# Kernel tuning notes

Hardware: AMD Instinct MI355X
Metric: run time of the kernel (lower is better)

## Reference

```python
import jax, jax.numpy as jnp
import numpy as np

N = 100000          # nodes
E = 1600000         # edges
NODE_DIM = 128
EDGE_DIM = 1
EMB = 16            # out_channels per head
H = 2               # heads
HID = 32
OUT = 2
NEG_SLOPE = 0.2


def gatv2_layer(x, src, dst, eattr, Wl, bl, Wr, br, We, att, bias):
    """PyG GATv2Conv: add self-loops (edge_attr fill='mean'), edge attention,
    segment softmax over target nodes, scatter-add aggregation, concat heads."""
    n = x.shape[0]
    heads, ch = att.shape
    # --- add self loops; self-loop edge_attr = mean of incoming edge_attr per node ---
    ones = jnp.ones((src.shape[0],), dtype=x.dtype)
    deg = jax.ops.segment_sum(ones, dst, num_segments=n)
    loop_attr = jax.ops.segment_sum(eattr, dst, num_segments=n) / jnp.maximum(deg, 1.0)[:, None]
    idx = jnp.arange(n, dtype=src.dtype)
    src2 = jnp.concatenate([src, idx])
    dst2 = jnp.concatenate([dst, idx])
    eattr2 = jnp.concatenate([eattr, loop_attr], axis=0)
    # --- linear projections ---
    xl = (x @ Wl + bl).reshape(n, heads, ch)   # source-side (lin_l)
    xr = (x @ Wr + br).reshape(n, heads, ch)   # target-side (lin_r)
    ef = (eattr2 @ We).reshape(-1, heads, ch)  # edge features (lin_edge, no bias)
    # --- per-edge attention logits (GATv2: LeakyReLU inside, then att dot) ---
    e = xl[src2] + xr[dst2] + ef               # [E2, H, C]
    e = jnp.where(e >= 0, e, NEG_SLOPE * e)
    logits = jnp.einsum('ehc,hc->eh', e, att)  # [E2, H]
    # --- segment softmax over edges sharing the same target node ---
    m = jax.ops.segment_max(logits, dst2, num_segments=n)      # [N, H]
    a = jnp.exp(logits - m[dst2])
    denom = jax.ops.segment_sum(a, dst2, num_segments=n)
    alpha = a / denom[dst2]                                    # [E2, H]
    # --- scatter-add weighted source messages ---
    msg = (alpha[:, :, None] * xl[src2]).reshape(-1, heads * ch)
    out = jax.ops.segment_sum(msg, dst2, num_segments=n)       # [N, H*C]
    return out + bias


def setup_inputs() -> dict:
    key = jax.random.key(0)
    ks = jax.random.split(key, 24)
    p = lambda k, s: (jax.random.normal(k, s, dtype=jnp.float32) * 0.1)
    HC = H * EMB
    return {
        'x': jax.random.normal(ks[0], (N, NODE_DIM), dtype=jnp.float32),
        'edge_index': jax.random.randint(ks[1], (2, E), 0, N, dtype=jnp.int32),
        'edge_attr': jax.random.normal(ks[2], (E, EDGE_DIM), dtype=jnp.float32),
        # layer 1
        'Wl1': p(ks[3], (NODE_DIM, HC)), 'bl1': p(ks[4], (HC,)),
        'Wr1': p(ks[5], (NODE_DIM, HC)), 'br1': p(ks[6], (HC,)),
        'We1': p(ks[7], (EDGE_DIM, HC)), 'att1': p(ks[8], (H, EMB)), 'b1': p(ks[9], (HC,)),
        # layer 2 (input dim = H*EMB)
        'Wl2': p(ks[10], (HC, HC)), 'bl2': p(ks[11], (HC,)),
        'Wr2': p(ks[12], (HC, HC)), 'br2': p(ks[13], (HC,)),
        'We2': p(ks[14], (EDGE_DIM, HC)), 'att2': p(ks[15], (H, EMB)), 'b2': p(ks[16], (HC,)),
        # decoder MLP
        'Wd1': p(ks[17], (HC, HID)), 'bd1': p(ks[18], (HID,)),
        'Wd2': p(ks[19], (HID, OUT)), 'bd2': p(ks[20], (OUT,)),
    }


def reference(x, edge_index, edge_attr,
              Wl1, bl1, Wr1, br1, We1, att1, b1,
              Wl2, bl2, Wr2, br2, We2, att2, b2,
              Wd1, bd1, Wd2, bd2):
    src, dst = edge_index[0], edge_index[1]
    h = gatv2_layer(x, src, dst, edge_attr, Wl1, bl1, Wr1, br1, We1, att1, b1)
    h = gatv2_layer(h, src, dst, edge_attr, Wl2, bl2, Wr2, br2, We2, att2, b2)
    h = jax.nn.relu(h @ Wd1 + bd1)
    return h @ Wd2 + bd2
```

## Files before the change

### kernel.cpp

```cpp
#include <hip/hip_runtime.h>
#include <hip/hip_fp16.h>
#include <math.h>


#define NN 100000
#define NE 1600000
#define SLOT 48
#define ROWU 64
#define NEG_SLOPE 0.2f

__global__ void scatter_kernel(const int* __restrict__ src, const int* __restrict__ dst,
                               const float* __restrict__ eattr,
                               unsigned* __restrict__ csr) {
    int e = blockIdx.x * blockDim.x + threadIdx.x;
    if (e >= NE) return;
    int d = dst[e];
    unsigned* row = csr + (size_t)d * ROWU;
    int pos = atomicAdd((int*)row, 1);
    if (pos < SLOT) {
        unsigned hb = __half_as_ushort(__float2half_rn(eattr[e]));
        row[4 + pos] = ((unsigned)src[e] << 15) | (hb >> 1);
    }
}

__device__ __forceinline__ int pk_src(unsigned p) { return (int)(p >> 15); }
__device__ __forceinline__ float pk_ea(unsigned p) {
    return __half2float(__ushort_as_half((unsigned short)((p & 0x7FFFu) << 1)));
}

template <int K>
__global__ void proj_kernel(const float* __restrict__ x,
                            const float* __restrict__ Wl, const float* __restrict__ bl,
                            const float* __restrict__ Wr, const float* __restrict__ br,
                            __half* __restrict__ xl, float* __restrict__ xr) {
    __shared__ float sWl[K * 32];
    __shared__ float sWr[K * 32];
    __shared__ float sb[64];
    for (int i = threadIdx.x; i < K * 32; i += blockDim.x) {
        sWl[i] = Wl[i];
        sWr[i] = Wr[i];
    }
    if (threadIdx.x < 32) sb[threadIdx.x] = bl[threadIdx.x];
    else if (threadIdx.x < 64) sb[threadIdx.x] = br[threadIdx.x - 32];
    __syncthreads();
    int t = blockIdx.x * blockDim.x + threadIdx.x;
    int g = t >> 5, col = t & 31;
    int row0 = g * 2;
    if (row0 >= NN) return;
    const float4* xr0 = (const float4*)(x + (size_t)row0 * K);
    const float4* xr1 = (const float4*)(x + (size_t)(row0 + 1) * K);
    float al0 = 0.f, ar0 = 0.f, al1 = 0.f, ar1 = 0.f;
#pragma unroll
    for (int k4 = 0; k4 < K / 4; k4++) {
        float4 a = xr0[k4];
        float4 b = xr1[k4];
        int k = k4 * 4;
        float wl0 = sWl[(k + 0) * 32 + col], wr0 = sWr[(k + 0) * 32 + col];
        float wl1 = sWl[(k + 1) * 32 + col], wr1 = sWr[(k + 1) * 32 + col];
        float wl2 = sWl[(k + 2) * 32 + col], wr2 = sWr[(k + 2) * 32 + col];
        float wl3 = sWl[(k + 3) * 32 + col], wr3 = sWr[(k + 3) * 32 + col];
        al0 = fmaf(a.x, wl0, al0); ar0 = fmaf(a.x, wr0, ar0);
        al1 = fmaf(b.x, wl0, al1); ar1 = fmaf(b.x, wr0, ar1);
        al0 = fmaf(a.y, wl1, al0); ar0 = fmaf(a.y, wr1, ar0);
        al1 = fmaf(b.y, wl1, al1); ar1 = fmaf(b.y, wr1, ar1);
        al0 = fmaf(a.z, wl2, al0); ar0 = fmaf(a.z, wr2, ar0);
        al1 = fmaf(b.z, wl2, al1); ar1 = fmaf(b.z, wr2, ar1);
        al0 = fmaf(a.w, wl3, al0); ar0 = fmaf(a.w, wr3, ar0);
        al1 = fmaf(b.w, wl3, al1); ar1 = fmaf(b.w, wr3, ar1);
    }
    xl[(size_t)row0 * 32 + col] = __float2half_rn(al0 + sb[col]);
    xr[(size_t)row0 * 32 + col] = ar0 + sb[32 + col];
    xl[(size_t)(row0 + 1) * 32 + col] = __float2half_rn(al1 + sb[col]);
    xr[(size_t)(row0 + 1) * 32 + col] = ar1 + sb[32 + col];
}

__device__ __forceinline__ float gat_core(const unsigned* csr,
                                          const __half* xl, const float* xr,
                                          const float* We, const float* att,
                                          const float* bias, int node, int c) {
    float we = We[c], at = att[c], bc = bias[c];
    float xrc = xr[(size_t)node * 32 + c];
    const unsigned* row = csr + (size_t)node * ROWU;
    int cnt = (int)row[0];
    int deg = (cnt < SLOT) ? cnt : SLOT;
    const unsigned* ep = row + 4;
    const uint4* ep4 = (const uint4*)ep;
    float ssum = 0.f, acc = 0.f, easum = 0.f;
    int k4 = deg >> 2;
    for (int kk = 0; kk < k4; kk++) {
        uint4 pv = ep4[kk];
        int s0 = pk_src(pv.x), s1 = pk_src(pv.y), s2 = pk_src(pv.z), s3 = pk_src(pv.w);
        float ea0 = pk_ea(pv.x), ea1 = pk_ea(pv.y), ea2 = pk_ea(pv.z), ea3 = pk_ea(pv.w);
        float xls0 = __half2float(xl[(size_t)s0 * 32 + c]);
        float xls1 = __half2float(xl[(size_t)s1 * 32 + c]);
        float xls2 = __half2float(xl[(size_t)s2 * 32 + c]);
        float xls3 = __half2float(xl[(size_t)s3 * 32 + c]);
        easum += (ea0 + ea1) + (ea2 + ea3);
        float v0 = xls0 + xrc + ea0 * we;
        float v1 = xls1 + xrc + ea1 * we;
        float v2 = xls2 + xrc + ea2 * we;
        float v3 = xls3 + xrc + ea3 * we;
        v0 = (v0 >= 0.f) ? v0 : NEG_SLOPE * v0;
        v1 = (v1 >= 0.f) ? v1 : NEG_SLOPE * v1;
        v2 = (v2 >= 0.f) ? v2 : NEG_SLOPE * v2;
        v3 = (v3 >= 0.f) ? v3 : NEG_SLOPE * v3;
        float p0 = v0 * at, p1 = v1 * at, p2 = v2 * at, p3 = v3 * at;
        p0 += __shfl_xor(p0, 1);  p1 += __shfl_xor(p1, 1);
        p2 += __shfl_xor(p2, 1);  p3 += __shfl_xor(p3, 1);
        p0 += __shfl_xor(p0, 2);  p1 += __shfl_xor(p1, 2);
        p2 += __shfl_xor(p2, 2);  p3 += __shfl_xor(p3, 2);
        p0 += __shfl_xor(p0, 4);  p1 += __shfl_xor(p1, 4);
        p2 += __shfl_xor(p2, 4);  p3 += __shfl_xor(p3, 4);
        p0 += __shfl_xor(p0, 8);  p1 += __shfl_xor(p1, 8);
        p2 += __shfl_xor(p2, 8);  p3 += __shfl_xor(p3, 8);
        float w0 = __expf(p0), w1 = __expf(p1), w2 = __expf(p2), w3 = __expf(p3);
        ssum += (w0 + w1) + (w2 + w3);
        acc = fmaf(w0, xls0, fmaf(w1, xls1, fmaf(w2, xls2, fmaf(w3, xls3, acc))));
    }
    for (int k = k4 * 4; k < deg; k++) {
        unsigned pv = ep[k];
        int s = pk_src(pv);
        float ea = pk_ea(pv);
        easum += ea;
        float xls = __half2float(xl[(size_t)s * 32 + c]);
        float v = xls + xrc + ea * we;
        v = (v >= 0.f) ? v : NEG_SLOPE * v;
        float p = v * at;
        p += __shfl_xor(p, 1);
        p += __shfl_xor(p, 2);
        p += __shfl_xor(p, 4);
        p += __shfl_xor(p, 8);
        float w = __expf(p);
        ssum += w;
        acc = fmaf(w, xls, acc);
    }
    {
        float ea0 = easum / fmaxf((float)cnt, 1.f);
        float xls0 = __half2float(xl[(size_t)node * 32 + c]);
        float v = xls0 + xrc + ea0 * we;
        v = (v >= 0.f) ? v : NEG_SLOPE * v;
        float p = v * at;
        p += __shfl_xor(p, 1);
        p += __shfl_xor(p, 2);
        p += __shfl_xor(p, 4);
        p += __shfl_xor(p, 8);
        float w = __expf(p);
        ssum += w;
        acc = fmaf(w, xls0, acc);
    }
    return acc / ssum + bc;
}

__global__ void gat1_proj2_kernel(const unsigned* __restrict__ csr,
                                  const __half* __restrict__ xl, const float* __restrict__ xr,
                                  const float* __restrict__ We, const float* __restrict__ att,
                                  const float* __restrict__ bias,
                                  const float* __restrict__ Wl2, const float* __restrict__ bl2,
                                  const float* __restrict__ Wr2, const float* __restrict__ br2,
                                  __half* __restrict__ xl2, float* __restrict__ xr2) {
    __shared__ float sWl[1024];
    __shared__ float sWr[1024];
    for (int i = threadIdx.x; i < 1024; i += blockDim.x) {
        sWl[i] = Wl2[i];
        sWr[i] = Wr2[i];
    }
    __syncthreads();
    int t = blockIdx.x * blockDim.x + threadIdx.x;
    int node = t >> 5, c = t & 31;
    if (node >= NN) return;
    float h = gat_core(csr, xl, xr, We, att, bias, node, c);
    float al = bl2[c], ar = br2[c];
#pragma unroll 8
    for (int cc = 0; cc < 32; cc++) {
        float bh = __shfl(h, cc, 32);
        al = fmaf(bh, sWl[cc * 32 + c], al);
        ar = fmaf(bh, sWr[cc * 32 + c], ar);
    }
    xl2[(size_t)node * 32 + c] = __float2half_rn(al);
    xr2[(size_t)node * 32 + c] = ar;
}

__global__ void gat2_dec_kernel(const unsigned* __restrict__ csr,
                                const __half* __restrict__ xl, const float* __restrict__ xr,
                                const float* __restrict__ We, const float* __restrict__ att,
                                const float* __restrict__ bias,
                                const float* __restrict__ Wd1, const float* __restrict__ bd1,
                                const float* __restrict__ Wd2, const float* __restrict__ bd2,
                                float* __restrict__ out) {
    __shared__ float sWd1[1024];
    __shared__ float sWd2[64];
    for (int i = threadIdx.x; i < 1024; i += blockDim.x) sWd1[i] = Wd1[i];
    if (threadIdx.x < 64) sWd2[threadIdx.x] = Wd2[threadIdx.x];
    __syncthreads();
    int t = blockIdx.x * blockDim.x + threadIdx.x;
    int node = t >> 5, c = t & 31;
    if (node >= NN) return;
    float h = gat_core(csr, xl, xr, We, att, bias, node, c);
    float d1 = bd1[c];
#pragma unroll 8
    for (int cc = 0; cc < 32; cc++) {
        float bh = __shfl(h, cc, 32);
        d1 = fmaf(bh, sWd1[cc * 32 + c], d1);
    }
    float hid = fmaxf(d1, 0.f);
    float o0 = hid * sWd2[c * 2 + 0];
    float o1 = hid * sWd2[c * 2 + 1];
    o0 += __shfl_xor(o0, 1);   o1 += __shfl_xor(o1, 1);
    o0 += __shfl_xor(o0, 2);   o1 += __shfl_xor(o1, 2);
    o0 += __shfl_xor(o0, 4);   o1 += __shfl_xor(o1, 4);
    o0 += __shfl_xor(o0, 8);   o1 += __shfl_xor(o1, 8);
    o0 += __shfl_xor(o0, 16);  o1 += __shfl_xor(o1, 16);
    if (c == 0) {
        out[(size_t)node * 2 + 0] = o0 + bd2[0];
        out[(size_t)node * 2 + 1] = o1 + bd2[1];
    }
}

extern "C" void kernel_launch(void* const* d_in, const int* in_sizes, int n_in,
                              void* d_out, int out_size, void* d_ws, size_t ws_size,
                              hipStream_t stream) {
    const float* x     = (const float*)d_in[0];
    const int*   src   = (const int*)d_in[1];
    const int*   dst   = src + NE;
    const float* eattr = (const float*)d_in[2];
    const float* Wl1 = (const float*)d_in[3],  *bl1 = (const float*)d_in[4];
    const float* Wr1 = (const float*)d_in[5],  *br1 = (const float*)d_in[6];
    const float* We1 = (const float*)d_in[7],  *att1 = (const float*)d_in[8];
    const float* b1  = (const float*)d_in[9];
    const float* Wl2 = (const float*)d_in[10], *bl2 = (const float*)d_in[11];
    const float* Wr2 = (const float*)d_in[12], *br2 = (const float*)d_in[13];
    const float* We2 = (const float*)d_in[14], *att2 = (const float*)d_in[15];
    const float* b2  = (const float*)d_in[16];
    const float* Wd1 = (const float*)d_in[17], *bd1 = (const float*)d_in[18];
    const float* Wd2 = (const float*)d_in[19], *bd2 = (const float*)d_in[20];
    float* out = (float*)d_out;

    char* w = (char*)d_ws;
    unsigned* csr = (unsigned*)w;  w += (size_t)NN * ROWU * 4;
    __half*   xl  = (__half*)w;    w += (size_t)NN * 32 * 2;
    float*    xr  = (float*)w;     w += (size_t)NN * 32 * 4;
    __half*   xl2 = (__half*)w;    w += (size_t)NN * 32 * 2;
    float*    xr2 = (float*)w;     w += (size_t)NN * 32 * 4;

    const int B = 256;
    const int gE   = NE / B;
    const int gN32 = (NN * 32) / B;
    const int gN16 = (NN / 2 * 32) / B;

    hipMemsetAsync(csr, 0, (size_t)NN * ROWU * 4, stream);
    scatter_kernel<<<gE, B, 0, stream>>>(src, dst, eattr, csr);

    proj_kernel<128><<<gN16, B, 0, stream>>>(x, Wl1, bl1, Wr1, br1, xl, xr);

    gat1_proj2_kernel<<<gN32, B, 0, stream>>>(csr, xl, xr, We1, att1, b1,
                                              Wl2, bl2, Wr2, br2, xl2, xr2);

    gat2_dec_kernel<<<gN32, B, 0, stream>>>(csr, xl2, xr2, We2, att2, b2,
                                            Wd1, bd1, Wd2, bd2, out);
}
```

Before: 432.5 us.

## Process four edges in parallel per node with 4-channel lanes in GAT aggregation

Rewrites the per-node attention aggregation so each lane handles four channels of one of four concurrent edges, instead of one channel of every edge in sequence. Gathers become 8-byte ushort4 loads, and the per-edge shuffle reduction drops from four steps to two. Partial sums are combined across edge groups with cross-lane shuffles at the end. The goal is fewer serial iterations and fewer shuffles per edge, at the cost of more registers and some lanes doing masked work on tail edges.

```diff
diff --git a/kernel.cpp b/kernel.cpp
--- a/kernel.cpp
+++ b/kernel.cpp
@@ -26,6 +26,9 @@
 __device__ __forceinline__ int pk_src(unsigned p) { return (int)(p >> 15); }
 __device__ __forceinline__ float pk_ea(unsigned p) {
     return __half2float(__ushort_as_half((unsigned short)((p & 0x7FFFu) << 1)));
+}
+__device__ __forceinline__ float lrelu(float v) {
+    return (v >= 0.f) ? v : NEG_SLOPE * v;
 }
 
 template <int K>
@@ -74,81 +77,78 @@
     xr[(size_t)(row0 + 1) * 32 + col] = ar1 + sb[32 + col];
 }
 
-__device__ __forceinline__ float gat_core(const unsigned* csr,
+__device__ __forceinline__ void gat_core4(const unsigned* csr,
                                           const __half* xl, const float* xr,
                                           const float* We, const float* att,
-                                          const float* bias, int node, int c) {
-    float we = We[c], at = att[c], bc = bias[c];
-    float xrc = xr[(size_t)node * 32 + c];
+                                          const float* bias, int node, int L,
+                                          float h[4]) {
+    int k = L & 7, j = L >> 3;
     const unsigned* row = csr + (size_t)node * ROWU;
     int cnt = (int)row[0];
     int deg = (cnt < SLOT) ? cnt : SLOT;
-    const unsigned* ep = row + 4;
-    const uint4* ep4 = (const uint4*)ep;
-    float ssum = 0.f, acc = 0.f, easum = 0.f;
-    int k4 = deg >> 2;
-    for (int kk = 0; kk < k4; kk++) {
-        uint4 pv = ep4[kk];
-        int s0 = pk_src(pv.x), s1 = pk_src(pv.y), s2 = pk_src(pv.z), s3 = pk_src(pv.w);
-        float ea0 = pk_ea(pv.x), ea1 = pk_ea(pv.y), ea2 = pk_ea(pv.z), ea3 = pk_ea(pv.w);
-        float xls0 = __half2float(xl[(size_t)s0 * 32 + c]);
-        float xls1 = __half2float(xl[(size_t)s1 * 32 + c]);
-        float xls2 = __half2float(xl[(size_t)s2 * 32 + c]);
-        float xls3 = __half2float(xl[(size_t)s3 * 32 + c]);
-        easum += (ea0 + ea1) + (ea2 + ea3);
-        float v0 = xls0 + xrc + ea0 * we;
-        float v1 = xls1 + xrc + ea1 * we;
-        float v2 = xls2 + xrc + ea2 * we;
-        float v3 = xls3 + xrc + ea3 * we;
-        v0 = (v0 >= 0.f) ? v0 : NEG_SLOPE * v0;
-        v1 = (v1 >= 0.f) ? v1 : NEG_SLOPE * v1;
-        v2 = (v2 >= 0.f) ? v2 : NEG_SLOPE * v2;
-        v3 = (v3 >= 0.f) ? v3 : NEG_SLOPE * v3;
-        float p0 = v0 * at, p1 = v1 * at, p2 = v2 * at, p3 = v3 * at;
-        p0 += __shfl_xor(p0, 1);  p1 += __shfl_xor(p1, 1);
-        p2 += __shfl_xor(p2, 1);  p3 += __shfl_xor(p3, 1);
-        p0 += __shfl_xor(p0, 2);  p1 += __shfl_xor(p1, 2);
-        p2 += __shfl_xor(p2, 2);  p3 += __shfl_xor(p3, 2);
-        p0 += __shfl_xor(p0, 4);  p1 += __shfl_xor(p1, 4);
-        p2 += __shfl_xor(p2, 4);  p3 += __shfl_xor(p3, 4);
-        p0 += __shfl_xor(p0, 8);  p1 += __shfl_xor(p1, 8);
-        p2 += __shfl_xor(p2, 8);  p3 += __shfl_xor(p3, 8);
-        float w0 = __expf(p0), w1 = __expf(p1), w2 = __expf(p2), w3 = __expf(p3);
-        ssum += (w0 + w1) + (w2 + w3);
-        acc = fmaf(w0, xls0, fmaf(w1, xls1, fmaf(w2, xls2, fmaf(w3, xls3, acc))));
-    }
-    for (int k = k4 * 4; k < deg; k++) {
-        unsigned pv = ep[k];
+    float4 we = ((const float4*)We)[k];
+    float4 at = ((const float4*)att)[k];
+    float4 xrc = ((const float4*)(xr + (size_t)node * 32))[k];
+    ushort4 sq = ((const ushort4*)(xl + (size_t)node * 32))[k];
+    float sx0 = __half2float(__ushort_as_half(sq.x));
+    float sx1 = __half2float(__ushort_as_half(sq.y));
+    float sx2 = __half2float(__ushort_as_half(sq.z));
+    float sx3 = __half2float(__ushort_as_half(sq.w));
+    float ssum = 0.f, a0 = 0.f, a1 = 0.f, a2 = 0.f, a3 = 0.f, easum = 0.f;
+    for (int base = 0; base < deg; base += 4) {
+        int idx = base + j;
+        unsigned pv = row[4 + idx];
         int s = pk_src(pv);
         float ea = pk_ea(pv);
-        easum += ea;
-        float xls = __half2float(xl[(size_t)s * 32 + c]);
-        float v = xls + xrc + ea * we;
-        v = (v >= 0.f) ? v : NEG_SLOPE * v;
-        float p = v * at;
+        ushort4 q = ((const ushort4*)(xl + (size_t)s * 32))[k];
+        float x0 = __half2float(__ushort_as_half(q.x));
+        float x1 = __half2float(__ushort_as_half(q.y));
+        float x2 = __half2float(__ushort_as_half(q.z));
+        float x3 = __half2float(__ushort_as_half(q.w));
+        float p;
+        p  = at.x * lrelu(fmaf(ea, we.x, x0 + xrc.x));
+        p  = fmaf(at.y, lrelu(fmaf(ea, we.y, x1 + xrc.y)), p);
+        p  = fmaf(at.z, lrelu(fmaf(ea, we.z, x2 + xrc.z)), p);
+        p  = fmaf(at.w, lrelu(fmaf(ea, we.w, x3 + xrc.w)), p);
         p += __shfl_xor(p, 1);
         p += __shfl_xor(p, 2);
-        p += __shfl_xor(p, 4);
-        p += __shfl_xor(p, 8);
+        bool valid = idx < deg;
+        float w = valid ? __expf(p) : 0.f;
+        ssum += w;
+        easum += valid ? ea : 0.f;
+        a0 = fmaf(w, x0, a0);
+        a1 = fmaf(w, x1, a1);
+        a2 = fmaf(w, x2, a2);
+        a3 = fmaf(w, x3, a3);
+    }
+    ssum  += __shfl_xor(ssum, 8);   ssum  += __shfl_xor(ssum, 16);
+    easum += __shfl_xor(easum, 8);  easum += __shfl_xor(easum, 16);
+    a0 += __shfl_xor(a0, 8);  a0 += __shfl_xor(a0, 16);
+    a1 += __shfl_xor(a1, 8);  a1 += __shfl_xor(a1, 16);
+    a2 += __shfl_xor(a2, 8);  a2 += __shfl_xor(a2, 16);
+    a3 += __shfl_xor(a3, 8);  a3 += __shfl_xor(a3, 16);
+    {
+        float ea0 = easum / fmaxf((float)cnt, 1.f);
+        float p;
+        p  = at.x * lrelu(fmaf(ea0, we.x, sx0 + xrc.x));
+        p  = fmaf(at.y, lrelu(fmaf(ea0, we.y, sx1 + xrc.y)), p);
+        p  = fmaf(at.z, lrelu(fmaf(ea0, we.z, sx2 + xrc.z)), p);
+        p  = fmaf(at.w, lrelu(fmaf(ea0, we.w, sx3 + xrc.w)), p);
+        p += __shfl_xor(p, 1);
+        p += __shfl_xor(p, 2);
         float w = __expf(p);
         ssum += w;
-        acc = fmaf(w, xls, acc);
-    }
-    {
-        float ea0 = easum / fmaxf((float)cnt, 1.f);
-        float xls0 = __half2float(xl[(size_t)node * 32 + c]);
-        float v = xls0 + xrc + ea0 * we;
-        v = (v >= 0.f) ? v : NEG_SLOPE * v;
-        float p = v * at;
-        p += __shfl_xor(p, 1);
-        p += __shfl_xor(p, 2);
-        p += __shfl_xor(p, 4);
-        p += __shfl_xor(p, 8);
-        float w = __expf(p);
-        ssum += w;
-        acc = fmaf(w, xls0, acc);
-    }
-    return acc / ssum + bc;
+        a0 = fmaf(w, sx0, a0);
+        a1 = fmaf(w, sx1, a1);
+        a2 = fmaf(w, sx2, a2);
+        a3 = fmaf(w, sx3, a3);
+    }
+    float4 bq = ((const float4*)bias)[k];
+    float inv = 1.f / ssum;
+    h[0] = a0 * inv + bq.x;
+    h[1] = a1 * inv + bq.y;
+    h[2] = a2 * inv + bq.z;
+    h[3] = a3 * inv + bq.w;
 }
 
 __global__ void gat1_proj2_kernel(const unsigned* __restrict__ csr,
@@ -166,18 +166,19 @@
     }
     __syncthreads();
     int t = blockIdx.x * blockDim.x + threadIdx.x;
-    int node = t >> 5, c = t & 31;
+    int node = t >> 5, L = t & 31;
     if (node >= NN) return;
-    float h = gat_core(csr, xl, xr, We, att, bias, node, c);
-    float al = bl2[c], ar = br2[c];
-#pragma unroll 8
+    float h[4];
+    gat_core4(csr, xl, xr, We, att, bias, node, L, h);
+    float al = bl2[L], ar = br2[L];
+#pragma unroll
     for (int cc = 0; cc < 32; cc++) {
-        float bh = __shfl(h, cc, 32);
-        al = fmaf(bh, sWl[cc * 32 + c], al);
-        ar = fmaf(bh, sWr[cc * 32 + c], ar);
-    }
-    xl2[(size_t)node * 32 + c] = __float2half_rn(al);
-    xr2[(size_t)node * 32 + c] = ar;
+        float bh = __shfl(h[cc & 3], cc >> 2, 8);
+        al = fmaf(bh, sWl[cc * 32 + L], al);
+        ar = fmaf(bh, sWr[cc * 32 + L], ar);
+    }
+    xl2[(size_t)node * 32 + L] = __float2half_rn(al);
+    xr2[(size_t)node * 32 + L] = ar;
 }
 
 __global__ void gat2_dec_kernel(const unsigned* __restrict__ csr,
@@ -193,24 +194,25 @@
     if (threadIdx.x < 64) sWd2[threadIdx.x] = Wd2[threadIdx.x];
     __syncthreads();
     int t = blockIdx.x * blockDim.x + threadIdx.x;
-    int node = t >> 5, c = t & 31;
+    int node = t >> 5, L = t & 31;
     if (node >= NN) return;
-    float h = gat_core(csr, xl, xr, We, att, bias, node, c);
-    float d1 = bd1[c];
-#pragma unroll 8
+    float h[4];
+    gat_core4(csr, xl, xr, We, att, bias, node, L, h);
+    float d1 = bd1[L];
+#pragma unroll
     for (int cc = 0; cc < 32; cc++) {
-        float bh = __shfl(h, cc, 32);
-        d1 = fmaf(bh, sWd1[cc * 32 + c], d1);
+        float bh = __shfl(h[cc & 3], cc >> 2, 8);
+        d1 = fmaf(bh, sWd1[cc * 32 + L], d1);
     }
     float hid = fmaxf(d1, 0.f);
-    float o0 = hid * sWd2[c * 2 + 0];
-    float o1 = hid * sWd2[c * 2 + 1];
+    float o0 = hid * sWd2[L * 2 + 0];
+    float o1 = hid * sWd2[L * 2 + 1];
     o0 += __shfl_xor(o0, 1);   o1 += __shfl_xor(o1, 1);
     o0 += __shfl_xor(o0, 2);   o1 += __shfl_xor(o1, 2);
     o0 += __shfl_xor(o0, 4);   o1 += __shfl_xor(o1, 4);
     o0 += __shfl_xor(o0, 8);   o1 += __shfl_xor(o1, 8);
     o0 += __shfl_xor(o0, 16);  o1 += __shfl_xor(o1, 16);
-    if (c == 0) {
+    if (L == 0) {
         out[(size_t)node * 2 + 0] = o0 + bd2[0];
         out[(size_t)node * 2 + 1] = o1 + bd2[1];
     }
```

Result: faster. 381.8 us (-11.7%).
